# Optimization experiments

Hardware: AMD Instinct MI355X
Metric: run time of the kernel (lower is better)

Reference implementation:

```python
import jax, jax.numpy as jnp
import numpy as np

B, S, H, F, E, K = 4, 2048, 1024, 3584, 8, 2


def setup_inputs() -> dict:
    key = jax.random.key(0)
    ks = jax.random.split(key, 5)
    sc = 0.02
    return {
        "hidden_states": jax.random.normal(ks[0], (B, S, H), jnp.float32),
        "router_w": jax.random.normal(ks[1], (E, H), jnp.float32) * sc,
        "w1": jax.random.normal(ks[2], (E, F, H), jnp.float32) * sc,
        "v1": jax.random.normal(ks[3], (E, F, H), jnp.float32) * sc,
        "w2": jax.random.normal(ks[4], (E, F, H), jnp.float32) * sc,
    }


def reference(hidden_states, router_w, w1, v1, w2):
    b, s, h = hidden_states.shape
    x = hidden_states.reshape(-1, h)  # [T, H] tokens (transpose(0,1) is a no-op per-token)
    T = x.shape[0]
    n_exp = w1.shape[0]

    # --- Mixtral router: fp32 softmax, top-k, renormalize ---
    logits = x @ router_w.T  # [T, E]
    scores = jax.nn.softmax(logits.astype(jnp.float32), axis=-1)
    expert_weights, expert_indices = jax.lax.top_k(scores, K)  # [T, K]
    expert_weights = expert_weights / expert_weights.sum(axis=-1, keepdims=True)
    expert_weights = expert_weights.astype(x.dtype)

    # combine coefficients: coef[t, e] = sum_k weight[t,k] * (idx[t,k]==e)
    coef = jnp.zeros((T, n_exp), x.dtype)
    coef = coef.at[jnp.arange(T)[:, None], expert_indices].add(expert_weights)

    out = jnp.zeros_like(x)
    for e in range(n_exp):  # small fixed expert count
        hmid = jax.nn.silu(x @ w1[e].T) * (x @ v1[e].T)  # [T, F]
        out = out + coef[:, e:e + 1] * (hmid @ w2[e])  # [T, H]
    return out.reshape(b, s, h)
```

## Files before the change

kernel.cpp:

```cpp
#include <hip/hip_runtime.h>
#include <cstdint>
#include <cstddef>

#define T_TOK 8192
#define H_DIM 1024
#define F_DIM 3584
#define E_NUM 8
#define MAX_ROWS 17408
#define MAX_TILES 136

typedef __bf16 bf16_t;
typedef bf16_t bf16x8 __attribute__((ext_vector_type(8)));
typedef bf16_t bf16x4 __attribute__((ext_vector_type(4)));
typedef float floatx4 __attribute__((ext_vector_type(4)));

typedef const __attribute__((address_space(1))) void* gas_ptr;
typedef __attribute__((address_space(3))) void* las_ptr;

__device__ __forceinline__ void async_copy16(const void* g, void* l) {
    __builtin_amdgcn_global_load_lds((gas_ptr)g, (las_ptr)l, 16, 0, 0);
}

#define WAIT_VM0() asm volatile("s_waitcnt vmcnt(0)" ::: "memory")
#define BAR() __builtin_amdgcn_s_barrier()

__global__ void cast_f32_to_bf16(const float* __restrict__ in, bf16_t* __restrict__ out, int n4) {
    int i = blockIdx.x * blockDim.x + threadIdx.x;
    if (i < n4) {
        const float4 v = ((const float4*)in)[i];
        bf16x4 o;
        o[0] = (bf16_t)v.x; o[1] = (bf16_t)v.y; o[2] = (bf16_t)v.z; o[3] = (bf16_t)v.w;
        ((bf16x4*)out)[i] = o;
    }
}

__global__ void transpose_cast_w2(const float* __restrict__ W2, bf16_t* __restrict__ W2T) {
    __shared__ bf16_t tile[32][34];
    const int e = blockIdx.z;
    const int f0 = blockIdx.x * 32;
    const int h0 = blockIdx.y * 32;
    const float* src = W2 + (size_t)e * F_DIM * H_DIM;
    bf16_t* dst = W2T + (size_t)e * H_DIM * F_DIM;
    const int tx = threadIdx.x;
    const int ty = threadIdx.y;
#pragma unroll
    for (int r = 0; r < 32; r += 8)
        tile[ty + r][tx] = (bf16_t)src[(size_t)(f0 + ty + r) * H_DIM + (h0 + tx)];
    __syncthreads();
#pragma unroll
    for (int r = 0; r < 32; r += 8)
        dst[(size_t)(h0 + ty + r) * F_DIM + (f0 + tx)] = tile[tx][ty + r];
}

__global__ void router_kernel(const float* __restrict__ X, const float* __restrict__ RW,
                              int* __restrict__ tok_e, float* __restrict__ tok_w) {
    const int lane = threadIdx.x & 63;
    const int wave = threadIdx.x >> 6;
    const int t = blockIdx.x * 4 + wave;
    const float* xp = X + (size_t)t * H_DIM;
    float xr[16];
#pragma unroll
    for (int j = 0; j < 16; ++j) xr[j] = xp[j * 64 + lane];
    float logits[E_NUM];
#pragma unroll
    for (int e = 0; e < E_NUM; ++e) {
        const float* rp = RW + e * H_DIM;
        float a = 0.f;
#pragma unroll
        for (int j = 0; j < 16; ++j) a += xr[j] * rp[j * 64 + lane];
#pragma unroll
        for (int s = 32; s; s >>= 1) a += __shfl_xor(a, s, 64);
        logits[e] = a;
    }
    if (lane == 0) {
        float mx = logits[0];
#pragma unroll
        for (int e = 1; e < E_NUM; ++e) mx = fmaxf(mx, logits[e]);
        float p[E_NUM], sum = 0.f;
#pragma unroll
        for (int e = 0; e < E_NUM; ++e) { p[e] = __expf(logits[e] - mx); sum += p[e]; }
#pragma unroll
        for (int e = 0; e < E_NUM; ++e) p[e] /= sum;
        int i0 = 0;
#pragma unroll
        for (int e = 1; e < E_NUM; ++e) if (p[e] > p[i0]) i0 = e;
        int i1 = (i0 == 0) ? 1 : 0;
#pragma unroll
        for (int e = 0; e < E_NUM; ++e) if (e != i0 && p[e] > p[i1]) i1 = e;
        const float s2 = p[i0] + p[i1];
        tok_e[t * 2 + 0] = i0; tok_w[t * 2 + 0] = p[i0] / s2;
        tok_e[t * 2 + 1] = i1; tok_w[t * 2 + 1] = p[i1] / s2;
    }
}

__global__ void build_assignments(const int* __restrict__ tok_e, const float* __restrict__ tok_w,
                                  int* __restrict__ asg_tok, float* __restrict__ asg_wt,
                                  int* __restrict__ tok_slot, int* __restrict__ tile_meta,
                                  int* __restrict__ n_tiles_out) {
    __shared__ int cnt[E_NUM];
    __shared__ int seg_start[E_NUM];
    __shared__ int seg_pad[E_NUM];
    const int tid = threadIdx.x;
    if (tid < E_NUM) cnt[tid] = 0;
    __syncthreads();
    for (int i = tid; i < T_TOK * 2; i += 1024) atomicAdd(&cnt[tok_e[i]], 1);
    __syncthreads();
    if (tid == 0) {
        int run = 0, nt = 0;
        for (int e = 0; e < E_NUM; ++e) {
            seg_start[e] = run;
            const int tiles = (cnt[e] + 127) >> 7;
            seg_pad[e] = tiles << 7;
            for (int j = 0; j < tiles; ++j) {
                tile_meta[nt * 2] = e;
                tile_meta[nt * 2 + 1] = run + j * 128;
                ++nt;
            }
            run += tiles << 7;
        }
        *n_tiles_out = nt;
    }
    __syncthreads();
    if (tid < E_NUM) cnt[tid] = 0;
    __syncthreads();
    for (int i = tid; i < T_TOK * 2; i += 1024) {
        const int e = tok_e[i];
        const int slot = atomicAdd(&cnt[e], 1);
        const int g = seg_start[e] + slot;
        asg_tok[g] = i >> 1;
        asg_wt[g] = tok_w[i];
        tok_slot[i] = g;
    }
    __syncthreads();
    for (int e = 0; e < E_NUM; ++e)
        for (int j = cnt[e] + tid; j < seg_pad[e]; j += 1024) {
            asg_tok[seg_start[e] + j] = -1;
            asg_wt[seg_start[e] + j] = 0.f;
        }
}


__global__ __launch_bounds__(256, 2)
void gemm1_glu(const bf16_t* __restrict__ X, const bf16_t* __restrict__ W1all,
               const bf16_t* __restrict__ V1all, const int* __restrict__ asg_tok,
               const float* __restrict__ asg_wt, const int* __restrict__ tile_meta,
               const int* __restrict__ n_tiles, bf16_t* __restrict__ Hmid) {
    const int lin = blockIdx.x + MAX_TILES * blockIdx.y;
    const int w = (lin & 7) * (MAX_TILES * 28 / 8) + (lin >> 3);
    const int tile = w % MAX_TILES;
    const int nb = w / MAX_TILES;
    if (tile >= *n_tiles) return;
    const int e = tile_meta[tile * 2];
    const int row0 = tile_meta[tile * 2 + 1];
    const bf16_t* W1 = W1all + (size_t)e * F_DIM * H_DIM;
    const bf16_t* V1 = V1all + (size_t)e * F_DIM * H_DIM;

    __shared__ __attribute__((aligned(16))) bf16_t As[2][128 * 32];
    __shared__ __attribute__((aligned(16))) bf16_t B1s[2][128 * 32];
    __shared__ __attribute__((aligned(16))) bf16_t B2s[2][128 * 32];
    const int tid = threadIdx.x;
    const int lane = tid & 63;
    const int wave = tid >> 6;
    const int n0 = nb * 128;
    const int wm = (wave >> 1) * 64;
    const int wn = (wave & 1) * 64;
    const int fr = lane & 15;
    const int q = lane >> 4;

    floatx4 acc1[4][4], acc2[4][4];
    const floatx4 zero = {0.f, 0.f, 0.f, 0.f};
#pragma unroll
    for (int a = 0; a < 4; ++a)
#pragma unroll
        for (int b = 0; b < 4; ++b) { acc1[a][b] = zero; acc2[a][b] = zero; }

    const int srow = tid >> 2;
    const int c = ((tid & 3) - ((tid >> 3) & 3)) & 3;
    const int scc = c * 8;
    const int ldsb0 = (tid & 192) * 16;
    const int ldsb1 = 4096 + ldsb0;

    int t0 = asg_tok[row0 + srow];      if (t0 < 0) t0 = 0;
    int t1 = asg_tok[row0 + 64 + srow]; if (t1 < 0) t1 = 0;
    const bf16_t* a0p = X + (size_t)t0 * H_DIM + scc;
    const bf16_t* a1p = X + (size_t)t1 * H_DIM + scc;
    const bf16_t* b1p0 = W1 + (size_t)(n0 + srow) * H_DIM + scc;
    const bf16_t* b1p1 = W1 + (size_t)(n0 + 64 + srow) * H_DIM + scc;
    const bf16_t* b2p0 = V1 + (size_t)(n0 + srow) * H_DIM + scc;
    const bf16_t* b2p1 = V1 + (size_t)(n0 + 64 + srow) * H_DIM + scc;

    const int NT = H_DIM / 32;

    async_copy16(a0p,  (char*)As[0]  + ldsb0);
    async_copy16(a1p,  (char*)As[0]  + ldsb1);
    async_copy16(b1p0, (char*)B1s[0] + ldsb0);
    async_copy16(b1p1, (char*)B1s[0] + ldsb1);
    async_copy16(b2p0, (char*)B2s[0] + ldsb0);
    async_copy16(b2p1, (char*)B2s[0] + ldsb1);
    WAIT_VM0();
    BAR();

    for (int t = 0; t < NT; ++t) {
        const int cur = t & 1;
        if (t + 1 < NT) {
            const int k = (t + 1) * 32;
            async_copy16(a0p + k,  (char*)As[cur ^ 1]  + ldsb0);
            async_copy16(a1p + k,  (char*)As[cur ^ 1]  + ldsb1);
            async_copy16(b1p0 + k, (char*)B1s[cur ^ 1] + ldsb0);
            async_copy16(b1p1 + k, (char*)B1s[cur ^ 1] + ldsb1);
            async_copy16(b2p0 + k, (char*)B2s[cur ^ 1] + ldsb0);
            async_copy16(b2p1 + k, (char*)B2s[cur ^ 1] + ldsb1);
        }
        __builtin_amdgcn_sched_barrier(0);

        const bf16_t* Ar  = As[cur];
        const bf16_t* B1r = B1s[cur];
        const bf16_t* B2r = B2s[cur];
        bf16x8 af[4], b1f[4], b2f[4];
#pragma unroll
        for (int mi = 0; mi < 4; ++mi) {
            const int r = wm + mi * 16 + fr;
            const int sl = (q + ((r >> 1) & 3)) & 3;
            af[mi] = *(const bf16x8*)&Ar[r * 32 + sl * 8];
        }
#pragma unroll
        for (int ni = 0; ni < 4; ++ni) {
            const int r = wn + ni * 16 + fr;
            const int sl = (q + ((r >> 1) & 3)) & 3;
            b1f[ni] = *(const bf16x8*)&B1r[r * 32 + sl * 8];
            b2f[ni] = *(const bf16x8*)&B2r[r * 32 + sl * 8];
        }
        __builtin_amdgcn_s_setprio(1);
#pragma unroll
        for (int mi = 0; mi < 4; ++mi)
#pragma unroll
            for (int ni = 0; ni < 4; ++ni) {
                acc1[mi][ni] = __builtin_amdgcn_mfma_f32_16x16x32_bf16(af[mi], b1f[ni], acc1[mi][ni], 0, 0, 0);
                acc2[mi][ni] = __builtin_amdgcn_mfma_f32_16x16x32_bf16(af[mi], b2f[ni], acc2[mi][ni], 0, 0, 0);
            }
        __builtin_amdgcn_s_setprio(0);
        if (t + 1 < NT) {
            WAIT_VM0();
            BAR();
        }
    }

#pragma unroll
    for (int mi = 0; mi < 4; ++mi) {
#pragma unroll
        for (int r = 0; r < 4; ++r) {
            const int gr = row0 + wm + mi * 16 + q * 4 + r;
            const float wt = asg_wt[gr];
            bf16_t* hp = Hmid + (size_t)gr * F_DIM + n0 + wn + fr;
#pragma unroll
            for (int ni = 0; ni < 4; ++ni) {
                const float s1 = acc1[mi][ni][r];
                const float s2 = acc2[mi][ni][r];
                const float val = (s1 / (1.f + __expf(-s1))) * s2 * wt;
                hp[ni * 16] = (bf16_t)val;
            }
        }
    }
}

__global__ __launch_bounds__(256, 2)
void gemm2_out(const bf16_t* __restrict__ Hmid, const bf16_t* __restrict__ W2Tall,
               const int* __restrict__ tile_meta, const int* __restrict__ n_tiles,
               float* __restrict__ Oasm) {
    const int lin = blockIdx.x + MAX_TILES * blockIdx.y;
    const int w = (lin & 7) * MAX_TILES + (lin >> 3);
    const int tile = w >> 3;
    const int n0 = (w & 7) * 128;
    if (tile >= *n_tiles) return;
    const int e = tile_meta[tile * 2];
    const int row0 = tile_meta[tile * 2 + 1];
    const bf16_t* W2T = W2Tall + (size_t)e * H_DIM * F_DIM;

    __shared__ __attribute__((aligned(16))) bf16_t As[2][128 * 32];
    __shared__ __attribute__((aligned(16))) bf16_t Bs[2][128 * 32];
    const int tid = threadIdx.x;
    const int lane = tid & 63;
    const int wave = tid >> 6;
    const int wm = (wave >> 1) * 64;
    const int wn = (wave & 1) * 64;
    const int fr = lane & 15;
    const int q = lane >> 4;

    floatx4 acc[4][4];
    const floatx4 zero = {0.f, 0.f, 0.f, 0.f};
#pragma unroll
    for (int a = 0; a < 4; ++a)
#pragma unroll
        for (int b = 0; b < 4; ++b) acc[a][b] = zero;

    const int srow = tid >> 2;
    const int c = ((tid & 3) - ((tid >> 3) & 3)) & 3;
    const int scc = c * 8;
    const int ldsb0 = (tid & 192) * 16;
    const int ldsb1 = 4096 + ldsb0;

    const bf16_t* a0p = Hmid + (size_t)(row0 + srow) * F_DIM + scc;
    const bf16_t* a1p = Hmid + (size_t)(row0 + 64 + srow) * F_DIM + scc;
    const bf16_t* b0p = W2T + (size_t)(n0 + srow) * F_DIM + scc;
    const bf16_t* b1p = W2T + (size_t)(n0 + 64 + srow) * F_DIM + scc;

    const int NT = F_DIM / 32;

    async_copy16(a0p, (char*)As[0] + ldsb0);
    async_copy16(a1p, (char*)As[0] + ldsb1);
    async_copy16(b0p, (char*)Bs[0] + ldsb0);
    async_copy16(b1p, (char*)Bs[0] + ldsb1);
    WAIT_VM0();
    BAR();

    for (int t = 0; t < NT; ++t) {
        const int cur = t & 1;
        if (t + 1 < NT) {
            const int k = (t + 1) * 32;
            async_copy16(a0p + k, (char*)As[cur ^ 1] + ldsb0);
            async_copy16(a1p + k, (char*)As[cur ^ 1] + ldsb1);
            async_copy16(b0p + k, (char*)Bs[cur ^ 1] + ldsb0);
            async_copy16(b1p + k, (char*)Bs[cur ^ 1] + ldsb1);
        }
        __builtin_amdgcn_sched_barrier(0);

        const bf16_t* Ar = As[cur];
        const bf16_t* Br = Bs[cur];
        bf16x8 af[4], bf[4];
#pragma unroll
        for (int mi = 0; mi < 4; ++mi) {
            const int r = wm + mi * 16 + fr;
            const int sl = (q + ((r >> 1) & 3)) & 3;
            af[mi] = *(const bf16x8*)&Ar[r * 32 + sl * 8];
        }
#pragma unroll
        for (int ni = 0; ni < 4; ++ni) {
            const int r = wn + ni * 16 + fr;
            const int sl = (q + ((r >> 1) & 3)) & 3;
            bf[ni] = *(const bf16x8*)&Br[r * 32 + sl * 8];
        }
        __builtin_amdgcn_s_setprio(1);
#pragma unroll
        for (int mi = 0; mi < 4; ++mi)
#pragma unroll
            for (int ni = 0; ni < 4; ++ni)
                acc[mi][ni] = __builtin_amdgcn_mfma_f32_16x16x32_bf16(af[mi], bf[ni], acc[mi][ni], 0, 0, 0);
        __builtin_amdgcn_s_setprio(0);
        if (t + 1 < NT) {
            WAIT_VM0();
            BAR();
        }
    }

#pragma unroll
    for (int mi = 0; mi < 4; ++mi) {
#pragma unroll
        for (int r = 0; r < 4; ++r) {
            const int gr = row0 + wm + mi * 16 + q * 4 + r;
            float* op = Oasm + (size_t)gr * H_DIM + n0 + wn + fr;
#pragma unroll
            for (int ni = 0; ni < 4; ++ni)
                op[ni * 16] = acc[mi][ni][r];
        }
    }
}

__global__ void combine_kernel(const float* __restrict__ Oasm, const int* __restrict__ tok_slot,
                               float* __restrict__ Out) {
    const int t = blockIdx.x;
    const int s0 = tok_slot[t * 2];
    const int s1 = tok_slot[t * 2 + 1];
    const float4 v0 = ((const float4*)(Oasm + (size_t)s0 * H_DIM))[threadIdx.x];
    const float4 v1 = ((const float4*)(Oasm + (size_t)s1 * H_DIM))[threadIdx.x];
    float4 o; o.x = v0.x + v1.x; o.y = v0.y + v1.y; o.z = v0.z + v1.z; o.w = v0.w + v1.w;
    ((float4*)(Out + (size_t)t * H_DIM))[threadIdx.x] = o;
}

extern "C" void kernel_launch(void* const* d_in, const int* in_sizes, int n_in,
                              void* d_out, int out_size, void* d_ws, size_t ws_size,
                              hipStream_t stream) {
    const float* x  = (const float*)d_in[0];
    const float* rw = (const float*)d_in[1];
    const float* w1 = (const float*)d_in[2];
    const float* v1 = (const float*)d_in[3];
    const float* w2 = (const float*)d_in[4];
    float* out = (float*)d_out;

    char* ws = (char*)d_ws;
    const size_t MB = 1024 * 1024;
    bf16_t* xb   = (bf16_t*)(ws + 0);
    bf16_t* w1b  = (bf16_t*)(ws + 16 * MB);
    bf16_t* v1b  = (bf16_t*)(ws + 72 * MB);
    bf16_t* hmid = (bf16_t*)(ws + 128 * MB);
    bf16_t* w2t  = (bf16_t*)(ws + 0);
    float*  oasm = (float*)(ws + 56 * MB);
    char* meta = ws + 128 * MB + (size_t)MAX_ROWS * F_DIM * 2;
    int*   asg_tok  = (int*)meta;                meta += MAX_ROWS * 4;
    float* asg_wt   = (float*)meta;              meta += MAX_ROWS * 4;
    int*   tok_slot = (int*)meta;                meta += T_TOK * 2 * 4;
    int*   tok_e    = (int*)meta;                meta += T_TOK * 2 * 4;
    float* tok_w    = (float*)meta;              meta += T_TOK * 2 * 4;
    int*   tile_meta = (int*)meta;               meta += MAX_TILES * 2 * 4;
    int*   n_tiles   = (int*)meta;               meta += 4;

    const int nx4 = T_TOK * H_DIM / 4;
    const int nw4 = E_NUM * F_DIM * H_DIM / 4;
    cast_f32_to_bf16<<<nx4 / 256, 256, 0, stream>>>(x, xb, nx4);
    cast_f32_to_bf16<<<nw4 / 256, 256, 0, stream>>>(w1, w1b, nw4);
    cast_f32_to_bf16<<<nw4 / 256, 256, 0, stream>>>(v1, v1b, nw4);
    router_kernel<<<T_TOK / 4, 256, 0, stream>>>(x, rw, tok_e, tok_w);
    build_assignments<<<1, 1024, 0, stream>>>(tok_e, tok_w, asg_tok, asg_wt,
                                              tok_slot, tile_meta, n_tiles);
    gemm1_glu<<<dim3(MAX_TILES, F_DIM / 128), 256, 0, stream>>>(
        xb, w1b, v1b, asg_tok, asg_wt, tile_meta, n_tiles, hmid);
    transpose_cast_w2<<<dim3(F_DIM / 32, H_DIM / 32, E_NUM), dim3(32, 8), 0, stream>>>(w2, w2t);
    gemm2_out<<<dim3(MAX_TILES, H_DIM / 128), 256, 0, stream>>>(
        hmid, w2t, tile_meta, n_tiles, oasm);
    combine_kernel<<<T_TOK, 256, 0, stream>>>(oasm, tok_slot, out);
}
```

Baseline: 921.9 us.

## Rewrite GLU GEMM with 256x256 tiles, interleaved W1/V1 weights and 8-wave pipeline

W1 and V1 are now cast into a single interleaved bf16 matrix in 16-row groups, so one B tile holds both gate and up projections. gemm1 moves to 256x256 tiles with 512 threads, 128KB of LDS, XOR-swizzled layout and a hand-scheduled multi-phase MFMA loop that stages loads and uses barriers between phases. The routing metadata now pads expert segments to 256 rows and emits separate tile lists for gemm1 (256-row tiles) and gemm2 (128-row tiles). The goal is more data reuse per loaded tile and better overlap of loads with MFMA work. The cost is more padding per expert, fewer concurrent blocks per CU from the large LDS footprint, and heavy register pressure.

```diff
diff --git a/kernel.cpp b/kernel.cpp
--- a/kernel.cpp
+++ b/kernel.cpp
@@ -6,8 +6,10 @@
 #define H_DIM 1024
 #define F_DIM 3584
 #define E_NUM 8
-#define MAX_ROWS 17408
-#define MAX_TILES 136
+#define MAX_ROWS 18432
+#define MAX_T256 72
+#define MAX_T128 144
+#define NB1 28
 
 typedef __bf16 bf16_t;
 typedef bf16_t bf16x8 __attribute__((ext_vector_type(8)));
@@ -21,6 +23,7 @@
     __builtin_amdgcn_global_load_lds((gas_ptr)g, (las_ptr)l, 16, 0, 0);
 }
 
+#define SB0() __builtin_amdgcn_sched_barrier(0)
 #define WAIT_VM0() asm volatile("s_waitcnt vmcnt(0)" ::: "memory")
 #define BAR() __builtin_amdgcn_s_barrier()
 
@@ -32,6 +35,25 @@
         o[0] = (bf16_t)v.x; o[1] = (bf16_t)v.y; o[2] = (bf16_t)v.z; o[3] = (bf16_t)v.w;
         ((bf16x4*)out)[i] = o;
     }
+}
+
+__global__ void cast_interleave_glu(const float* __restrict__ W1, const float* __restrict__ V1,
+                                    bf16_t* __restrict__ Bcat, int n4) {
+    int i = blockIdx.x * blockDim.x + threadIdx.x;
+    if (i >= n4) return;
+    const int HQ = H_DIM / 4;
+    const int h4 = i & (HQ - 1);
+    const int rest = i >> 8;
+    const int f = rest % F_DIM;
+    const int e = rest / F_DIM;
+    const size_t dst = ((size_t)e * (2 * F_DIM) + 32 * (f >> 4) + (f & 15)) * H_DIM + h4 * 4;
+    const float4 a = ((const float4*)W1)[i];
+    const float4 b = ((const float4*)V1)[i];
+    bf16x4 oa, ob;
+    oa[0] = (bf16_t)a.x; oa[1] = (bf16_t)a.y; oa[2] = (bf16_t)a.z; oa[3] = (bf16_t)a.w;
+    ob[0] = (bf16_t)b.x; ob[1] = (bf16_t)b.y; ob[2] = (bf16_t)b.z; ob[3] = (bf16_t)b.w;
+    *(bf16x4*)(Bcat + dst) = oa;
+    *(bf16x4*)(Bcat + dst + (size_t)16 * H_DIM) = ob;
 }
 
 __global__ void transpose_cast_w2(const float* __restrict__ W2, bf16_t* __restrict__ W2T) {
@@ -95,8 +117,9 @@
 
 __global__ void build_assignments(const int* __restrict__ tok_e, const float* __restrict__ tok_w,
                                   int* __restrict__ asg_tok, float* __restrict__ asg_wt,
-                                  int* __restrict__ tok_slot, int* __restrict__ tile_meta,
-                                  int* __restrict__ n_tiles_out) {
+                                  int* __restrict__ tok_slot,
+                                  int* __restrict__ tm256, int* __restrict__ n256,
+                                  int* __restrict__ tm128, int* __restrict__ n128) {
     __shared__ int cnt[E_NUM];
     __shared__ int seg_start[E_NUM];
     __shared__ int seg_pad[E_NUM];
@@ -106,19 +129,16 @@
     for (int i = tid; i < T_TOK * 2; i += 1024) atomicAdd(&cnt[tok_e[i]], 1);
     __syncthreads();
     if (tid == 0) {
-        int run = 0, nt = 0;
+        int run = 0, a = 0, b = 0;
         for (int e = 0; e < E_NUM; ++e) {
             seg_start[e] = run;
-            const int tiles = (cnt[e] + 127) >> 7;
-            seg_pad[e] = tiles << 7;
-            for (int j = 0; j < tiles; ++j) {
-                tile_meta[nt * 2] = e;
-                tile_meta[nt * 2 + 1] = run + j * 128;
-                ++nt;
-            }
-            run += tiles << 7;
-        }
-        *n_tiles_out = nt;
+            const int t256 = (cnt[e] + 255) >> 8;
+            seg_pad[e] = t256 << 8;
+            for (int j = 0; j < t256; ++j) { tm256[a * 2] = e; tm256[a * 2 + 1] = run + j * 256; ++a; }
+            for (int j = 0; j < t256 * 2; ++j) { tm128[b * 2] = e; tm128[b * 2 + 1] = run + j * 128; ++b; }
+            run += t256 << 8;
+        }
+        *n256 = a; *n128 = b;
     }
     __syncthreads();
     if (tid < E_NUM) cnt[tid] = 0;
@@ -139,136 +159,169 @@
         }
 }
 
-
-__global__ __launch_bounds__(256, 2)
-void gemm1_glu(const bf16_t* __restrict__ X, const bf16_t* __restrict__ W1all,
-               const bf16_t* __restrict__ V1all, const int* __restrict__ asg_tok,
-               const float* __restrict__ asg_wt, const int* __restrict__ tile_meta,
-               const int* __restrict__ n_tiles, bf16_t* __restrict__ Hmid) {
-    const int lin = blockIdx.x + MAX_TILES * blockIdx.y;
-    const int w = (lin & 7) * (MAX_TILES * 28 / 8) + (lin >> 3);
-    const int tile = w % MAX_TILES;
-    const int nb = w / MAX_TILES;
+__global__ __launch_bounds__(512, 2)
+void gemm1_glu(const bf16_t* __restrict__ X, const bf16_t* __restrict__ Bcat,
+               const int* __restrict__ asg_tok, const float* __restrict__ asg_wt,
+               const int* __restrict__ tile_meta, const int* __restrict__ n_tiles,
+               bf16_t* __restrict__ Hmid) {
+    const int lin = blockIdx.x + MAX_T256 * blockIdx.y;
+    const int w = (lin & 7) * (MAX_T256 * NB1 / 8) + (lin >> 3);
+    const int tile = w % MAX_T256;
+    const int nb = w / MAX_T256;
     if (tile >= *n_tiles) return;
     const int e = tile_meta[tile * 2];
     const int row0 = tile_meta[tile * 2 + 1];
-    const bf16_t* W1 = W1all + (size_t)e * F_DIM * H_DIM;
-    const bf16_t* V1 = V1all + (size_t)e * F_DIM * H_DIM;
-
-    __shared__ __attribute__((aligned(16))) bf16_t As[2][128 * 32];
-    __shared__ __attribute__((aligned(16))) bf16_t B1s[2][128 * 32];
-    __shared__ __attribute__((aligned(16))) bf16_t B2s[2][128 * 32];
+
+    __shared__ __attribute__((aligned(16))) char lds[131072];
+
     const int tid = threadIdx.x;
     const int lane = tid & 63;
     const int wave = tid >> 6;
-    const int n0 = nb * 128;
-    const int wm = (wave >> 1) * 64;
-    const int wn = (wave & 1) * 64;
+    const int wm = wave >> 2;
+    const int wn = wave & 3;
     const int fr = lane & 15;
     const int q = lane >> 4;
 
-    floatx4 acc1[4][4], acc2[4][4];
+    const int srow = tid >> 3;
+    const int cA = (tid & 7) ^ (srow & 7);
+    const int ldsWave = wave * 1024;
+
+    const bf16_t* pA[4];
+    const bf16_t* pB[4];
+#pragma unroll
+    for (int j = 0; j < 4; ++j) {
+        int t = asg_tok[row0 + j * 64 + srow]; if (t < 0) t = 0;
+        pA[j] = X + (size_t)t * H_DIM + cA * 8;
+        pB[j] = Bcat + ((size_t)e * (2 * F_DIM) + (size_t)(nb * 256 + j * 64 + srow)) * H_DIM + cA * 8;
+    }
+
+#define STG_A(slot, half, ktEl) do { \
+    async_copy16(pA[(half)*2+0] + (ktEl), lds + (slot)*32768 + (half)*16384 + ldsWave); \
+    async_copy16(pA[(half)*2+1] + (ktEl), lds + (slot)*32768 + (half)*16384 + 8192 + ldsWave); \
+  } while (0)
+#define STG_B(slot, half, ktEl) do { \
+    async_copy16(pB[(half)*2+0] + (ktEl), lds + 65536 + (slot)*32768 + (half)*16384 + ldsWave); \
+    async_copy16(pB[(half)*2+1] + (ktEl), lds + 65536 + (slot)*32768 + (half)*16384 + 8192 + ldsWave); \
+  } while (0)
+
+    const int aRow = wm * 16384 + fr * 128;
+    const int bRow = 65536 + (wn >> 1) * 16384 + ((wn & 1) * 64 + fr) * 128;
+    int cOff[2];
+    cOff[0] = ((0 * 4 + q) ^ (fr & 7)) << 4;
+    cOff[1] = ((1 * 4 + q) ^ (fr & 7)) << 4;
+
+#define LDA(slot, mi, ks) (*(const bf16x8*)(lds + (slot)*32768 + aRow + (mi)*2048 + cOff[ks]))
+#define LDB(slot, ni, ks) (*(const bf16x8*)(lds + (slot)*32768 + bRow + (ni)*2048 + cOff[ks]))
+
+    floatx4 acc[8][4];
     const floatx4 zero = {0.f, 0.f, 0.f, 0.f};
 #pragma unroll
-    for (int a = 0; a < 4; ++a)
-#pragma unroll
-        for (int b = 0; b < 4; ++b) { acc1[a][b] = zero; acc2[a][b] = zero; }
-
-    const int srow = tid >> 2;
-    const int c = ((tid & 3) - ((tid >> 3) & 3)) & 3;
-    const int scc = c * 8;
-    const int ldsb0 = (tid & 192) * 16;
-    const int ldsb1 = 4096 + ldsb0;
-
-    int t0 = asg_tok[row0 + srow];      if (t0 < 0) t0 = 0;
-    int t1 = asg_tok[row0 + 64 + srow]; if (t1 < 0) t1 = 0;
-    const bf16_t* a0p = X + (size_t)t0 * H_DIM + scc;
-    const bf16_t* a1p = X + (size_t)t1 * H_DIM + scc;
-    const bf16_t* b1p0 = W1 + (size_t)(n0 + srow) * H_DIM + scc;
-    const bf16_t* b1p1 = W1 + (size_t)(n0 + 64 + srow) * H_DIM + scc;
-    const bf16_t* b2p0 = V1 + (size_t)(n0 + srow) * H_DIM + scc;
-    const bf16_t* b2p1 = V1 + (size_t)(n0 + 64 + srow) * H_DIM + scc;
-
-    const int NT = H_DIM / 32;
-
-    async_copy16(a0p,  (char*)As[0]  + ldsb0);
-    async_copy16(a1p,  (char*)As[0]  + ldsb1);
-    async_copy16(b1p0, (char*)B1s[0] + ldsb0);
-    async_copy16(b1p1, (char*)B1s[0] + ldsb1);
-    async_copy16(b2p0, (char*)B2s[0] + ldsb0);
-    async_copy16(b2p1, (char*)B2s[0] + ldsb1);
-    WAIT_VM0();
-    BAR();
-
-    for (int t = 0; t < NT; ++t) {
-        const int cur = t & 1;
-        if (t + 1 < NT) {
-            const int k = (t + 1) * 32;
-            async_copy16(a0p + k,  (char*)As[cur ^ 1]  + ldsb0);
-            async_copy16(a1p + k,  (char*)As[cur ^ 1]  + ldsb1);
-            async_copy16(b1p0 + k, (char*)B1s[cur ^ 1] + ldsb0);
-            async_copy16(b1p1 + k, (char*)B1s[cur ^ 1] + ldsb1);
-            async_copy16(b2p0 + k, (char*)B2s[cur ^ 1] + ldsb0);
-            async_copy16(b2p1 + k, (char*)B2s[cur ^ 1] + ldsb1);
-        }
-        __builtin_amdgcn_sched_barrier(0);
-
-        const bf16_t* Ar  = As[cur];
-        const bf16_t* B1r = B1s[cur];
-        const bf16_t* B2r = B2s[cur];
-        bf16x8 af[4], b1f[4], b2f[4];
-#pragma unroll
-        for (int mi = 0; mi < 4; ++mi) {
-            const int r = wm + mi * 16 + fr;
-            const int sl = (q + ((r >> 1) & 3)) & 3;
-            af[mi] = *(const bf16x8*)&Ar[r * 32 + sl * 8];
-        }
-#pragma unroll
-        for (int ni = 0; ni < 4; ++ni) {
-            const int r = wn + ni * 16 + fr;
-            const int sl = (q + ((r >> 1) & 3)) & 3;
-            b1f[ni] = *(const bf16x8*)&B1r[r * 32 + sl * 8];
-            b2f[ni] = *(const bf16x8*)&B2r[r * 32 + sl * 8];
-        }
-        __builtin_amdgcn_s_setprio(1);
-#pragma unroll
-        for (int mi = 0; mi < 4; ++mi)
-#pragma unroll
-            for (int ni = 0; ni < 4; ++ni) {
-                acc1[mi][ni] = __builtin_amdgcn_mfma_f32_16x16x32_bf16(af[mi], b1f[ni], acc1[mi][ni], 0, 0, 0);
-                acc2[mi][ni] = __builtin_amdgcn_mfma_f32_16x16x32_bf16(af[mi], b2f[ni], acc2[mi][ni], 0, 0, 0);
+    for (int m = 0; m < 8; ++m)
+#pragma unroll
+        for (int n = 0; n < 4; ++n) acc[m][n] = zero;
+
+    bf16x8 a[8], bn0[4], bn1[4];
+
+#define PH_PRE() do { SB0(); BAR(); \
+    asm volatile("s_waitcnt lgkmcnt(0)" ::: "memory"); SB0(); } while (0)
+#define PH_POST() do { SB0(); BAR(); SB0(); } while (0)
+#define MF16(mq, nq, BREG) do { \
+    __builtin_amdgcn_s_setprio(1); \
+    _Pragma("unroll") for (int ml = 0; ml < 4; ++ml) \
+    _Pragma("unroll") for (int nl = 0; nl < 2; ++nl) \
+    _Pragma("unroll") for (int ks = 0; ks < 2; ++ks) \
+        acc[(mq)*4+ml][(nq)*2+nl] = __builtin_amdgcn_mfma_f32_16x16x32_bf16( \
+            a[ml*2+ks], BREG[nl*2+ks], acc[(mq)*4+ml][(nq)*2+nl], 0, 0, 0); \
+    __builtin_amdgcn_s_setprio(0); \
+  } while (0)
+
+    STG_B(0, 0, 0); STG_B(0, 1, 0); STG_A(0, 0, 0); STG_A(0, 1, 0);
+    STG_B(1, 0, 64); STG_B(1, 1, 64); STG_A(1, 0, 64); STG_A(1, 1, 64);
+    asm volatile("s_waitcnt vmcnt(8)" ::: "memory");
+    BAR(); SB0();
+
+#pragma unroll 1
+    for (int i = 0; i < 8; ++i) {
+        const bool stg = (i < 7);
+        const int k0e = (2 * i + 2) * 64;
+        const int k1e = k0e + 64;
+
+#pragma unroll
+        for (int ml = 0; ml < 4; ++ml) { a[ml*2+0] = LDA(0, ml, 0); a[ml*2+1] = LDA(0, ml, 1); }
+#pragma unroll
+        for (int nl = 0; nl < 2; ++nl) { bn0[nl*2+0] = LDB(0, nl, 0); bn0[nl*2+1] = LDB(0, nl, 1); }
+        PH_PRE(); MF16(0, 0, bn0); PH_POST();
+
+#pragma unroll
+        for (int nl = 0; nl < 2; ++nl) { bn1[nl*2+0] = LDB(0, 2+nl, 0); bn1[nl*2+1] = LDB(0, 2+nl, 1); }
+        PH_PRE(); MF16(0, 1, bn1); PH_POST();
+
+        if (stg) STG_B(0, 0, k0e);
+#pragma unroll
+        for (int ml = 0; ml < 4; ++ml) { a[ml*2+0] = LDA(0, 4+ml, 0); a[ml*2+1] = LDA(0, 4+ml, 1); }
+        PH_PRE(); MF16(1, 0, bn0); PH_POST();
+
+        if (stg) STG_B(0, 1, k0e);
+        PH_PRE(); MF16(1, 1, bn1);
+        SB0();
+        if (stg) asm volatile("s_waitcnt vmcnt(4)" ::: "memory");
+        else     asm volatile("s_waitcnt vmcnt(0)" ::: "memory");
+        BAR(); SB0();
+
+        if (stg) STG_A(0, 0, k0e);
+#pragma unroll
+        for (int ml = 0; ml < 4; ++ml) { a[ml*2+0] = LDA(1, ml, 0); a[ml*2+1] = LDA(1, ml, 1); }
+#pragma unroll
+        for (int nl = 0; nl < 2; ++nl) { bn0[nl*2+0] = LDB(1, nl, 0); bn0[nl*2+1] = LDB(1, nl, 1); }
+        PH_PRE(); MF16(0, 0, bn0); PH_POST();
+
+        if (stg) STG_A(0, 1, k0e);
+#pragma unroll
+        for (int nl = 0; nl < 2; ++nl) { bn1[nl*2+0] = LDB(1, 2+nl, 0); bn1[nl*2+1] = LDB(1, 2+nl, 1); }
+        PH_PRE(); MF16(0, 1, bn1); PH_POST();
+
+        if (stg) { STG_B(1, 0, k1e); STG_B(1, 1, k1e); }
+#pragma unroll
+        for (int ml = 0; ml < 4; ++ml) { a[ml*2+0] = LDA(1, 4+ml, 0); a[ml*2+1] = LDA(1, 4+ml, 1); }
+        PH_PRE(); MF16(1, 0, bn0); PH_POST();
+
+        if (stg) { STG_A(1, 0, k1e); STG_A(1, 1, k1e); }
+        PH_PRE(); MF16(1, 1, bn1);
+        SB0();
+        asm volatile("s_waitcnt vmcnt(8)" ::: "memory");
+        BAR(); SB0();
+    }
+
+#pragma unroll
+    for (int mi = 0; mi < 8; ++mi) {
+#pragma unroll
+        for (int rr = 0; rr < 4; ++rr) {
+            const int gr = row0 + wm * 128 + mi * 16 + q * 4 + rr;
+            const float wt = asg_wt[gr];
+            bf16_t* hp = Hmid + (size_t)gr * F_DIM + nb * 128 + (2 * wn) * 16 + fr;
+#pragma unroll
+            for (int fb = 0; fb < 2; ++fb) {
+                const float s1 = acc[mi][2 * fb][rr];
+                const float s2 = acc[mi][2 * fb + 1][rr];
+                hp[fb * 16] = (bf16_t)((s1 / (1.f + __expf(-s1))) * s2 * wt);
             }
-        __builtin_amdgcn_s_setprio(0);
-        if (t + 1 < NT) {
-            WAIT_VM0();
-            BAR();
-        }
-    }
-
-#pragma unroll
-    for (int mi = 0; mi < 4; ++mi) {
-#pragma unroll
-        for (int r = 0; r < 4; ++r) {
-            const int gr = row0 + wm + mi * 16 + q * 4 + r;
-            const float wt = asg_wt[gr];
-            bf16_t* hp = Hmid + (size_t)gr * F_DIM + n0 + wn + fr;
-#pragma unroll
-            for (int ni = 0; ni < 4; ++ni) {
-                const float s1 = acc1[mi][ni][r];
-                const float s2 = acc2[mi][ni][r];
-                const float val = (s1 / (1.f + __expf(-s1))) * s2 * wt;
-                hp[ni * 16] = (bf16_t)val;
-            }
-        }
-    }
+        }
+    }
+#undef STG_A
+#undef STG_B
+#undef LDA
+#undef LDB
+#undef PH_PRE
+#undef PH_POST
+#undef MF16
 }
 
 __global__ __launch_bounds__(256, 2)
 void gemm2_out(const bf16_t* __restrict__ Hmid, const bf16_t* __restrict__ W2Tall,
                const int* __restrict__ tile_meta, const int* __restrict__ n_tiles,
                float* __restrict__ Oasm) {
-    const int lin = blockIdx.x + MAX_TILES * blockIdx.y;
-    const int w = (lin & 7) * MAX_TILES + (lin >> 3);
+    const int lin = blockIdx.x + MAX_T128 * blockIdx.y;
+    const int w = (lin & 7) * MAX_T128 + (lin >> 3);
     const int tile = w >> 3;
     const int n0 = (w & 7) * 128;
     if (tile >= *n_tiles) return;
@@ -389,8 +442,7 @@
     char* ws = (char*)d_ws;
     const size_t MB = 1024 * 1024;
     bf16_t* xb   = (bf16_t*)(ws + 0);
-    bf16_t* w1b  = (bf16_t*)(ws + 16 * MB);
-    bf16_t* v1b  = (bf16_t*)(ws + 72 * MB);
+    bf16_t* bcat = (bf16_t*)(ws + 16 * MB);
     bf16_t* hmid = (bf16_t*)(ws + 128 * MB);
     bf16_t* w2t  = (bf16_t*)(ws + 0);
     float*  oasm = (float*)(ws + 56 * MB);
@@ -400,21 +452,21 @@
     int*   tok_slot = (int*)meta;                meta += T_TOK * 2 * 4;
     int*   tok_e    = (int*)meta;                meta += T_TOK * 2 * 4;
     float* tok_w    = (float*)meta;              meta += T_TOK * 2 * 4;
-    int*   tile_meta = (int*)meta;               meta += MAX_TILES * 2 * 4;
-    int*   n_tiles   = (int*)meta;               meta += 4;
+    int*   tm256    = (int*)meta;                meta += MAX_T256 * 2 * 4;
+    int*   n256     = (int*)meta;                meta += 4;
+    int*   tm128    = (int*)meta;                meta += MAX_T128 * 2 * 4;
+    int*   n128     = (int*)meta;                meta += 4;
 
     const int nx4 = T_TOK * H_DIM / 4;
     const int nw4 = E_NUM * F_DIM * H_DIM / 4;
     cast_f32_to_bf16<<<nx4 / 256, 256, 0, stream>>>(x, xb, nx4);
-    cast_f32_to_bf16<<<nw4 / 256, 256, 0, stream>>>(w1, w1b, nw4);
-    cast_f32_to_bf16<<<nw4 / 256, 256, 0, stream>>>(v1, v1b, nw4);
+    cast_interleave_glu<<<nw4 / 256, 256, 0, stream>>>(w1, v1, bcat, nw4);
     router_kernel<<<T_TOK / 4, 256, 0, stream>>>(x, rw, tok_e, tok_w);
-    build_assignments<<<1, 1024, 0, stream>>>(tok_e, tok_w, asg_tok, asg_wt,
-                                              tok_slot, tile_meta, n_tiles);
-    gemm1_glu<<<dim3(MAX_TILES, F_DIM / 128), 256, 0, stream>>>(
-        xb, w1b, v1b, asg_tok, asg_wt, tile_meta, n_tiles, hmid);
+    build_assignments<<<1, 1024, 0, stream>>>(tok_e, tok_w, asg_tok, asg_wt, tok_slot,
+                                              tm256, n256, tm128, n128);
+    gemm1_glu<<<dim3(MAX_T256, NB1), 512, 0, stream>>>(
+        xb, bcat, asg_tok, asg_wt, tm256, n256, hmid);
     transpose_cast_w2<<<dim3(F_DIM / 32, H_DIM / 32, E_NUM), dim3(32, 8), 0, stream>>>(w2, w2t);
-    gemm2_out<<<dim3(MAX_TILES, H_DIM / 128), 256, 0, stream>>>(
-        hmid, w2t, tile_meta, n_tiles, oasm);
+    gemm2_out<<<dim3(MAX_T128, 8), 256, 0, stream>>>(hmid, w2t, tm128, n128, oasm);
     combine_kernel<<<T_TOK, 256, 0, stream>>>(oasm, tok_slot, out);
 }
```

Result: faster. 889.9 us (-3.5%).
